# Kernel tuning notes

Measured on AMD Instinct MI355X. Metric: run time of the kernel, lower is better.

Reference implementation:

```python
import jax, jax.numpy as jnp
import numpy as np

B, S, I, H = 64, 512, 1024, 1024


def setup_inputs() -> dict:
    key = jax.random.key(0)
    ks = jax.random.split(key, 7)
    sc = 0.02
    return {
        "x": jax.random.normal(ks[0], (B, S, I), jnp.float32),
        "Wx0": jax.random.normal(ks[1], (I, 4 * H), jnp.float32) * sc,
        "Wh0": jax.random.normal(ks[2], (H, 4 * H), jnp.float32) * sc,
        "b0": jax.random.normal(ks[3], (4 * H,), jnp.float32) * sc,
        "Wx1": jax.random.normal(ks[4], (H, 4 * H), jnp.float32) * sc,
        "Wh1": jax.random.normal(ks[5], (H, 4 * H), jnp.float32) * sc,
        "b1": jax.random.normal(ks[6], (4 * H,), jnp.float32) * sc,
    }


def _lstm_layer(x_seq, Wx, Wh, b):
    """x_seq: (S, B, in). Gate order along 4H axis: i, f, g, o."""
    hid = Wh.shape[0]
    # Precompute input-side projections for all timesteps (one big GEMM).
    xg = jnp.einsum('sbi,ih->sbh', x_seq, Wx) + b  # (S, B, 4H)

    def step(carry, xg_t):
        h, c = carry
        g = xg_t + h @ Wh                      # (B, 4H)
        i, f, gg, o = jnp.split(g, 4, axis=-1)
        i = jax.nn.sigmoid(i)
        f = jax.nn.sigmoid(f)
        gg = jnp.tanh(gg)
        o = jax.nn.sigmoid(o)
        c = f * c + i * gg
        h = o * jnp.tanh(c)
        return (h, c), h

    bsz = x_seq.shape[1]
    h0 = jnp.zeros((bsz, hid), x_seq.dtype)
    c0 = jnp.zeros((bsz, hid), x_seq.dtype)
    (_, _), hs = jax.lax.scan(step, (h0, c0), xg)
    return hs  # (S, B, H)


def reference(x, Wx0, Wh0, b0, Wx1, Wh1, b1):
    # batch_first=True -> (B,S,I); internal layout is time-major (S,B,I)
    xs = jnp.swapaxes(x, 0, 1)
    h1 = _lstm_layer(xs, Wx0, Wh0, b0)
    h2 = _lstm_layer(h1, Wx1, Wh1, b1)
    return jnp.swapaxes(h2, 0, 1)  # (B, S, H)
```

## Files before the change

kernel.cpp:

```cpp
#include <hip/hip_runtime.h>
#include <hip/hip_bf16.h>

#define SEQ  512
#define HID  1024
#define G4   4096
#define NBLK 128

typedef short bf16x8 __attribute__((ext_vector_type(8)));
typedef float f32x4  __attribute__((ext_vector_type(4)));
typedef unsigned long long u64;

static __device__ __forceinline__ unsigned short f2b(float f) {
  union { float f; unsigned u; } v; v.f = f;
  unsigned r = (v.u + 0x7FFFu + ((v.u >> 16) & 1u)) >> 16;
  return (unsigned short)r;
}

__global__ __launch_bounds__(256) void k_castx(const float* __restrict__ x,
                                               unsigned short* __restrict__ xb) {
  int idx = blockIdx.x * 256 + threadIdx.x;
  int r = idx >> 8, kq = idx & 255;
  int b = r & 63, s = r >> 6;
  float4 v = *reinterpret_cast<const float4*>(x + ((size_t)b * SEQ + s) * HID + (size_t)kq * 4);
  ushort4 o;
  o.x = f2b(v.x); o.y = f2b(v.y); o.z = f2b(v.z); o.w = f2b(v.w);
  *reinterpret_cast<ushort4*>(xb + (size_t)r * HID + kq * 4) = o;
}

__global__ __launch_bounds__(256) void k_wtrans(const float* __restrict__ W,
                                                unsigned short* __restrict__ WT) {
  __shared__ float tls[32][33];
  int tile = blockIdx.x;
  int nt = tile & 127, kt = tile >> 7;
  int tx = threadIdx.x & 31, ty = threadIdx.x >> 5;
  int k0 = kt * 32, n0 = nt * 32;
  for (int i = 0; i < 4; ++i)
    tls[ty + 8 * i][tx] = W[(size_t)(k0 + ty + 8 * i) * G4 + n0 + tx];
  __syncthreads();
  for (int i = 0; i < 4; ++i)
    WT[(size_t)(n0 + ty + 8 * i) * HID + k0 + tx] = f2b(tls[tx][ty + 8 * i]);
}

static __device__ __forceinline__ void poll_flags128(unsigned* flags, unsigned tgt) {
  const int l = threadIdx.x & 63;
  unsigned* p0 = flags + l * 32;
  unsigned* p1 = flags + (64 + l) * 32;
  long sp = 0;
  for (;;) {
    unsigned v0 = __hip_atomic_load(p0, __ATOMIC_RELAXED, __HIP_MEMORY_SCOPE_AGENT);
    unsigned v1 = __hip_atomic_load(p1, __ATOMIC_RELAXED, __HIP_MEMORY_SCOPE_AGENT);
    if (__all((v0 >= tgt) && (v1 >= tgt))) break;
    if (++sp > 2000000L) break;
    __builtin_amdgcn_s_sleep(1);
  }
  asm volatile("" ::: "memory");
}

static __device__ __forceinline__ void lds_wait(int* f, int tgt) {
  long sp = 0;
  while (__hip_atomic_load(f, __ATOMIC_RELAXED, __HIP_MEMORY_SCOPE_WORKGROUP) < tgt) {
    if (++sp > 50000000L) break;
    __builtin_amdgcn_s_sleep(1);
  }
  asm volatile("" ::: "memory");
}

__global__ __launch_bounds__(512, 1) void k_scan2(
    const unsigned short* __restrict__ xb,
    const unsigned short* __restrict__ WxT0, const unsigned short* __restrict__ WhT0,
    const float* __restrict__ b0,
    const unsigned short* __restrict__ WxT1, const unsigned short* __restrict__ WhT1,
    const float* __restrict__ b1,
    unsigned short* __restrict__ h1,
    unsigned short* __restrict__ h2, int h2mod,
    float* __restrict__ out,
    unsigned* __restrict__ bars) {
  __shared__ unsigned short wlds[32 * 2048];
  __shared__ float x_lds[2][4][8][64];
  __shared__ unsigned lds_arr;
  __shared__ int hrdy, xrdy;

  const int bk  = blockIdx.x;
  const int layer = bk >> 7;
  const int nb  = bk & 127;
  const int tid = threadIdx.x;
  const int w   = tid >> 6;
  const int l   = tid & 63;
  const int lq  = l >> 4, lr = l & 15;
  const int rt  = w & 3;
  const bool is_h = (w >= 4);

  const unsigned short* WxT = layer ? WxT1 : WxT0;
  const unsigned short* WhT = layer ? WhT1 : WhT0;
  const float* bias = layer ? b1 : b0;
  const unsigned short* aseq = layer ? h1 : xb;
  unsigned short* hout = layer ? h2 : h1;
  const int hmod = layer ? h2mod : 512;
  float* fout = layer ? out : nullptr;
  unsigned* ownflags = bars + layer * 4096;
  unsigned* l0flags  = bars;
  unsigned* myflag   = ownflags + nb * 32;

  if (tid == 0) { lds_arr = 0; hrdy = 0; xrdy = 0; }

  {
    int c = tid >> 4, seg = tid & 15;
    int gate = c >> 3, nl = c & 7;
    int gcol = gate * 1024 + nb * 8 + nl;
    const unsigned short* sx = WxT + (size_t)gcol * HID;
    const unsigned short* sh = WhT + (size_t)gcol * HID;
    for (int j = 0; j < 16; ++j) {
      int kk = seg * 128 + j * 8;
      const unsigned short* src = (kk < 1024) ? (sx + kk) : (sh + kk - 1024);
      uint4 v = *reinterpret_cast<const uint4*>(src);
      int db = (c * 4096 + kk * 2) ^ ((c & 7) << 4);
      *reinterpret_cast<uint4*>(reinterpret_cast<char*>(wlds) + db) = v;
    }
  }

  char* wbase = reinterpret_cast<char*>(wlds);
  const int csw = (lr & 7) << 4;
  const int cb0 = (lr) * 4096 + lq * 16;
  const int cb1 = (16 + lr) * 4096 + lq * 16;

  float bias_c[2];
#pragma unroll
  for (int ct = 0; ct < 2; ++ct) {
    int col = ct * 16 + lr;
    bias_c[ct] = bias[(col >> 3) * 1024 + nb * 8 + (col & 7)];
  }

  float cst[4] = {0.f, 0.f, 0.f, 0.f};

  __syncthreads();
  if (is_h) __builtin_amdgcn_s_setprio(1);

  if (!is_h) {
    if (layer) poll_flags128(l0flags, 1u);
    const bf16x8* ax = reinterpret_cast<const bf16x8*>(aseq) + (size_t)(rt * 16 + lr) * 128 + lq;
    f32x4 acc[2][4] = {};
#pragma unroll 8
    for (int ks = 0; ks < 32; ++ks) {
      bf16x8 a  = ax[ks * 4];
      bf16x8 bb0 = *reinterpret_cast<const bf16x8*>(wbase + ((cb0 + ks * 64) ^ csw));
      bf16x8 bb1 = *reinterpret_cast<const bf16x8*>(wbase + ((cb1 + ks * 64) ^ csw));
      acc[0][ks & 3] = __builtin_amdgcn_mfma_f32_16x16x32_bf16(a, bb0, acc[0][ks & 3], 0, 0, 0);
      acc[1][ks & 3] = __builtin_amdgcn_mfma_f32_16x16x32_bf16(a, bb1, acc[1][ks & 3], 0, 0, 0);
    }
#pragma unroll
    for (int ct = 0; ct < 2; ++ct) {
      f32x4 s = (acc[ct][0] + acc[ct][1]) + (acc[ct][2] + acc[ct][3]);
      float bc = bias_c[ct];
      x_lds[0][w][ct * 4 + 0][l] = s.x + bc;
      x_lds[0][w][ct * 4 + 1][l] = s.y + bc;
      x_lds[0][w][ct * 4 + 2][l] = s.z + bc;
      x_lds[0][w][ct * 4 + 3][l] = s.w + bc;
    }
  }
  __syncthreads();

  for (int t = 0; t < SEQ; ++t) {
    if (!is_h) {
      if (t + 1 < SEQ) {
        if (layer) {
          if (w == 0) {
            poll_flags128(l0flags, (unsigned)(t + 2));
            __hip_atomic_store(&xrdy, t + 1, __ATOMIC_RELAXED, __HIP_MEMORY_SCOPE_WORKGROUP);
          } else {
            lds_wait(&xrdy, t + 1);
          }
        }
        const bf16x8* ax = reinterpret_cast<const bf16x8*>(aseq)
                           + ((size_t)(t + 1) * 64 + rt * 16 + lr) * 128 + lq;
        f32x4 acc[2][4] = {};
#pragma unroll 8
        for (int ks = 0; ks < 32; ++ks) {
          bf16x8 a  = ax[ks * 4];
          bf16x8 bb0 = *reinterpret_cast<const bf16x8*>(wbase + ((cb0 + ks * 64) ^ csw));
          bf16x8 bb1 = *reinterpret_cast<const bf16x8*>(wbase + ((cb1 + ks * 64) ^ csw));
          acc[0][ks & 3] = __builtin_amdgcn_mfma_f32_16x16x32_bf16(a, bb0, acc[0][ks & 3], 0, 0, 0);
          acc[1][ks & 3] = __builtin_amdgcn_mfma_f32_16x16x32_bf16(a, bb1, acc[1][ks & 3], 0, 0, 0);
        }
        int bn2 = (t + 1) & 1;
#pragma unroll
        for (int ct = 0; ct < 2; ++ct) {
          f32x4 s = (acc[ct][0] + acc[ct][1]) + (acc[ct][2] + acc[ct][3]);
          float bc = bias_c[ct];
          x_lds[bn2][w][ct * 4 + 0][l] = s.x + bc;
          x_lds[bn2][w][ct * 4 + 1][l] = s.y + bc;
          x_lds[bn2][w][ct * 4 + 2][l] = s.z + bc;
          x_lds[bn2][w][ct * 4 + 3][l] = s.w + bc;
        }
      }
    } else {
      const int bn = t & 1;
      f32x4 acc[2][4];
#pragma unroll
      for (int ct = 0; ct < 2; ++ct) {
        acc[ct][0] = f32x4{x_lds[bn][rt][ct * 4 + 0][l], x_lds[bn][rt][ct * 4 + 1][l],
                           x_lds[bn][rt][ct * 4 + 2][l], x_lds[bn][rt][ct * 4 + 3][l]};
        acc[ct][1] = f32x4{0.f, 0.f, 0.f, 0.f};
        acc[ct][2] = f32x4{0.f, 0.f, 0.f, 0.f};
        acc[ct][3] = f32x4{0.f, 0.f, 0.f, 0.f};
      }

      if (t > 0) {
        if (w == 4) {
          poll_flags128(ownflags, (unsigned)t);
          __hip_atomic_store(&hrdy, t, __ATOMIC_RELAXED, __HIP_MEMORY_SCOPE_WORKGROUP);
        } else {
          lds_wait(&hrdy, t);
        }
        const size_t hbase = (size_t)((t - 1) % hmod) * (64 * HID) + (size_t)(rt * 16 + lr) * HID;
        if (hmod != 4) {
          const bf16x8* hp = reinterpret_cast<const bf16x8*>(hout + hbase) + lq;
#pragma unroll 8
          for (int ks = 0; ks < 32; ++ks) {
            bf16x8 a = hp[ks * 4];
            bf16x8 bb0 = *reinterpret_cast<const bf16x8*>(wbase + ((cb0 + 2048 + ks * 64) ^ csw));
            bf16x8 bb1 = *reinterpret_cast<const bf16x8*>(wbase + ((cb1 + 2048 + ks * 64) ^ csw));
            acc[0][ks & 3] = __builtin_amdgcn_mfma_f32_16x16x32_bf16(a, bb0, acc[0][ks & 3], 0, 0, 0);
            acc[1][ks & 3] = __builtin_amdgcn_mfma_f32_16x16x32_bf16(a, bb1, acc[1][ks & 3], 0, 0, 0);
          }
        } else {
          const u64* hp = reinterpret_cast<const u64*>(hout + hbase) + lq * 2;
#pragma unroll 8
          for (int ks = 0; ks < 32; ++ks) {
            u64 q0 = __hip_atomic_load(hp + ks * 8,     __ATOMIC_RELAXED, __HIP_MEMORY_SCOPE_AGENT);
            u64 q1 = __hip_atomic_load(hp + ks * 8 + 1, __ATOMIC_RELAXED, __HIP_MEMORY_SCOPE_AGENT);
            union { u64 q[2]; bf16x8 v; } u; u.q[0] = q0; u.q[1] = q1;
            bf16x8 bb0 = *reinterpret_cast<const bf16x8*>(wbase + ((cb0 + 2048 + ks * 64) ^ csw));
            bf16x8 bb1 = *reinterpret_cast<const bf16x8*>(wbase + ((cb1 + 2048 + ks * 64) ^ csw));
            acc[0][ks & 3] = __builtin_amdgcn_mfma_f32_16x16x32_bf16(u.v, bb0, acc[0][ks & 3], 0, 0, 0);
            acc[1][ks & 3] = __builtin_amdgcn_mfma_f32_16x16x32_bf16(u.v, bb1, acc[1][ks & 3], 0, 0, 0);
          }
        }
      }

      f32x4 s0 = (acc[0][0] + acc[0][1]) + (acc[0][2] + acc[0][3]);
      f32x4 s1 = (acc[1][0] + acc[1][1]) + (acc[1][2] + acc[1][3]);
      float a0[4] = {s0.x, s0.y, s0.z, s0.w};
      float a1[4] = {s1.x, s1.y, s1.z, s1.w};
      float b0r[4], b1r[4];
#pragma unroll
      for (int r = 0; r < 4; ++r) {
        b0r[r] = __shfl_xor(a0[r], 8, 64);
        b1r[r] = __shfl_xor(a1[r], 8, 64);
      }
      const bool isX = ((l & 8) == 0);
      float hvf[4];
#pragma unroll
      for (int r = 0; r < 4; ++r) {
        float gi = isX ? a0[r] : b0r[r];
        float gf = isX ? b0r[r] : a0[r];
        float gg = isX ? a1[r] : b1r[r];
        float go = isX ? b1r[r] : a1[r];
        float ig = 1.f / (1.f + __expf(-gi));
        float fg = 1.f / (1.f + __expf(-gf));
        float e2 = __expf(2.f * gg);
        float gv = (e2 - 1.f) / (e2 + 1.f);
        float og = 1.f / (1.f + __expf(-go));
        cst[r] = fg * cst[r] + ig * gv;
        float e2c = __expf(2.f * cst[r]);
        hvf[r] = og * (e2c - 1.f) / (e2c + 1.f);
      }
      float hn[4];
#pragma unroll
      for (int r = 0; r < 4; ++r) hn[r] = __shfl_xor(hvf[r], 1, 64);
      const bool ev = ((l & 1) == 0);
      unsigned pk[4]; float he[4], ho[4];
#pragma unroll
      for (int r = 0; r < 4; ++r) {
        he[r] = ev ? hvf[r] : hn[r];
        ho[r] = ev ? hn[r] : hvf[r];
        pk[r] = (unsigned)f2b(he[r]) | ((unsigned)f2b(ho[r]) << 16);
      }
      const int sub = ((l >> 3) & 1) * 2 + (l & 1);
      unsigned pks = sub == 0 ? pk[0] : sub == 1 ? pk[1] : sub == 2 ? pk[2] : pk[3];
      const int row = rt * 16 + lq * 4 + sub;
      const int cp  = (lr & 7) >> 1;
      unsigned* hw = reinterpret_cast<unsigned*>(hout + (size_t)(t % hmod) * (64 * HID))
                     + (size_t)row * 512 + nb * 4 + cp;
      __hip_atomic_store(hw, pks, __ATOMIC_RELAXED, __HIP_MEMORY_SCOPE_AGENT);

      asm volatile("s_waitcnt vmcnt(0)" ::: "memory");
      if (l == 0) {
        atomicAdd(&lds_arr, 1u);
        if (w == 4) {
          long sp = 0;
          while (__hip_atomic_load(&lds_arr, __ATOMIC_RELAXED, __HIP_MEMORY_SCOPE_WORKGROUP)
                 < 4u * (unsigned)(t + 1)) {
            if (++sp > 50000000L) break;
            __builtin_amdgcn_s_sleep(1);
          }
          __hip_atomic_store(myflag, (unsigned)(t + 1), __ATOMIC_RELAXED, __HIP_MEMORY_SCOPE_AGENT);
        }
      }

      if (fout) {
        float hes = sub == 0 ? he[0] : sub == 1 ? he[1] : sub == 2 ? he[2] : he[3];
        float hos = sub == 0 ? ho[0] : sub == 1 ? ho[1] : sub == 2 ? ho[2] : ho[3];
        *reinterpret_cast<float2*>(fout + (size_t)row * (SEQ * HID) + (size_t)t * HID
                                   + nb * 8 + cp * 2) = make_float2(hes, hos);
      }
    }
    __syncthreads();
  }
}

extern "C" void kernel_launch(void* const* d_in, const int* in_sizes, int n_in,
                              void* d_out, int out_size, void* d_ws, size_t ws_size,
                              hipStream_t stream) {
  const float* x   = (const float*)d_in[0];
  const float* Wx0 = (const float*)d_in[1];
  const float* Wh0 = (const float*)d_in[2];
  const float* b0  = (const float*)d_in[3];
  const float* Wx1 = (const float*)d_in[4];
  const float* Wh1 = (const float*)d_in[5];
  const float* b1  = (const float*)d_in[6];
  float* out = (float*)d_out;
  char* ws = (char*)d_ws;

  unsigned short* xb   = (unsigned short*)(ws);
  unsigned short* h1   = (unsigned short*)(ws + 67108864);
  unsigned short* WxT0 = (unsigned short*)(ws + 134217728);
  unsigned short* WhT0 = (unsigned short*)(ws + 142606336);
  unsigned short* WxT1 = (unsigned short*)(ws + 150994944);
  unsigned short* WhT1 = (unsigned short*)(ws + 159383552);
  unsigned* bars       = (unsigned*)(ws + 167772160);
  unsigned short* h2   = (unsigned short*)(ws + 167804928);
  int h2mod = (ws_size >= (size_t)167804928 + 67108864) ? 512 : 4;

  hipMemsetAsync(bars, 0, 32768, stream);
  k_castx<<<32768, 256, 0, stream>>>(x, xb);
  k_wtrans<<<4096, 256, 0, stream>>>(Wx0, WxT0);
  k_wtrans<<<4096, 256, 0, stream>>>(Wh0, WhT0);
  k_wtrans<<<4096, 256, 0, stream>>>(Wx1, WxT1);
  k_wtrans<<<4096, 256, 0, stream>>>(Wh1, WhT1);
  k_scan2<<<2 * NBLK, 512, 0, stream>>>(xb, WxT0, WhT0, b0, WxT1, WhT1, b1,
                                        h1, h2, h2mod, out, bars);
}
```

Baseline: 4.788 ms.

## Retile recurrent MFMA per wave and move output stores to x-projection waves

Each wave now computes 32 batch rows by 16 gate columns instead of 16 rows by 32 columns. The weight columns in LDS are interleaved by gate, so the i/f/g/o values for a hidden unit sit in adjacent lanes and are gathered with xor-1/xor-2 shuffles. This halves the LDS weight reads per k-step but doubles the global reads of the h operand on the recurrent critical path. The fp32 output stores are taken off the h-waves: the x-projection waves re-read the previous step's bf16 h from global memory and write it out. As a result the output now carries bf16-rounded values.

New measurement: 8.915 ms. 1.86x slower.

```diff
diff --git a/kernel.cpp b/kernel.cpp
--- a/kernel.cpp
+++ b/kernel.cpp
@@ -14,6 +14,12 @@
   union { float f; unsigned u; } v; v.f = f;
   unsigned r = (v.u + 0x7FFFu + ((v.u >> 16) & 1u)) >> 16;
   return (unsigned short)r;
+}
+static __device__ __forceinline__ float b2f_lo(unsigned u) {
+  union { unsigned u; float f; } v; v.u = u << 16; return v.f;
+}
+static __device__ __forceinline__ float b2f_hi(unsigned u) {
+  union { unsigned u; float f; } v; v.u = u & 0xFFFF0000u; return v.f;
 }
 
 __global__ __launch_bounds__(256) void k_castx(const float* __restrict__ x,
@@ -87,7 +93,8 @@
   const int w   = tid >> 6;
   const int l   = tid & 63;
   const int lq  = l >> 4, lr = l & 15;
-  const int rt  = w & 3;
+  const int rt2 = (w >> 1) & 1;
+  const int ct  = w & 1;
   const bool is_h = (w >= 4);
 
   const unsigned short* WxT = layer ? WxT1 : WxT0;
@@ -105,8 +112,8 @@
 
   {
     int c = tid >> 4, seg = tid & 15;
-    int gate = c >> 3, nl = c & 7;
-    int gcol = gate * 1024 + nb * 8 + nl;
+    int gate = c & 3, hcl = c >> 2;
+    int gcol = gate * 1024 + nb * 8 + hcl;
     const unsigned short* sx = WxT + (size_t)gcol * HID;
     const unsigned short* sh = WhT + (size_t)gcol * HID;
     for (int j = 0; j < 16; ++j) {
@@ -119,48 +126,55 @@
   }
 
   char* wbase = reinterpret_cast<char*>(wlds);
-  const int csw = (lr & 7) << 4;
-  const int cb0 = (lr) * 4096 + lq * 16;
-  const int cb1 = (16 + lr) * 4096 + lq * 16;
-
-  float bias_c[2];
-#pragma unroll
-  for (int ct = 0; ct < 2; ++ct) {
-    int col = ct * 16 + lr;
-    bias_c[ct] = bias[(col >> 3) * 1024 + nb * 8 + (col & 7)];
-  }
-
-  float cst[4] = {0.f, 0.f, 0.f, 0.f};
+  const int c_w = ct * 16 + lr;
+  const int csw = (c_w & 7) << 4;
+  const int cb  = c_w * 4096 + lq * 16;
+  const int gate = lr & 3;
+  const int hcl  = ct * 4 + (lr >> 2);
+  const float bias_c = bias[gate * 1024 + nb * 8 + hcl];
+
+  float cst[8] = {0.f};
 
   __syncthreads();
   if (is_h) __builtin_amdgcn_s_setprio(1);
 
   if (!is_h) {
     if (layer) poll_flags128(l0flags, 1u);
-    const bf16x8* ax = reinterpret_cast<const bf16x8*>(aseq) + (size_t)(rt * 16 + lr) * 128 + lq;
+    const bf16x8* ax0 = reinterpret_cast<const bf16x8*>(aseq)
+                        + (size_t)(rt2 * 32 + lr) * 128 + lq;
+    const bf16x8* ax1 = ax0 + 16 * 128;
     f32x4 acc[2][4] = {};
 #pragma unroll 8
     for (int ks = 0; ks < 32; ++ks) {
-      bf16x8 a  = ax[ks * 4];
-      bf16x8 bb0 = *reinterpret_cast<const bf16x8*>(wbase + ((cb0 + ks * 64) ^ csw));
-      bf16x8 bb1 = *reinterpret_cast<const bf16x8*>(wbase + ((cb1 + ks * 64) ^ csw));
-      acc[0][ks & 3] = __builtin_amdgcn_mfma_f32_16x16x32_bf16(a, bb0, acc[0][ks & 3], 0, 0, 0);
-      acc[1][ks & 3] = __builtin_amdgcn_mfma_f32_16x16x32_bf16(a, bb1, acc[1][ks & 3], 0, 0, 0);
+      bf16x8 a0 = ax0[ks * 4];
+      bf16x8 a1 = ax1[ks * 4];
+      bf16x8 bb = *reinterpret_cast<const bf16x8*>(wbase + ((cb + ks * 64) ^ csw));
+      acc[0][ks & 3] = __builtin_amdgcn_mfma_f32_16x16x32_bf16(a0, bb, acc[0][ks & 3], 0, 0, 0);
+      acc[1][ks & 3] = __builtin_amdgcn_mfma_f32_16x16x32_bf16(a1, bb, acc[1][ks & 3], 0, 0, 0);
     }
 #pragma unroll
-    for (int ct = 0; ct < 2; ++ct) {
-      f32x4 s = (acc[ct][0] + acc[ct][1]) + (acc[ct][2] + acc[ct][3]);
-      float bc = bias_c[ct];
-      x_lds[0][w][ct * 4 + 0][l] = s.x + bc;
-      x_lds[0][w][ct * 4 + 1][l] = s.y + bc;
-      x_lds[0][w][ct * 4 + 2][l] = s.z + bc;
-      x_lds[0][w][ct * 4 + 3][l] = s.w + bc;
+    for (int ar = 0; ar < 2; ++ar) {
+      f32x4 s = (acc[ar][0] + acc[ar][1]) + (acc[ar][2] + acc[ar][3]);
+      x_lds[0][w][ar * 4 + 0][l] = s.x + bias_c;
+      x_lds[0][w][ar * 4 + 1][l] = s.y + bias_c;
+      x_lds[0][w][ar * 4 + 2][l] = s.z + bias_c;
+      x_lds[0][w][ar * 4 + 3][l] = s.w + bias_c;
     }
   }
   __syncthreads();
 
   for (int t = 0; t < SEQ; ++t) {
     if (!is_h) {
+      if (fout && t > 0) {
+        int tc = t - 1;
+        const unsigned* sp32 = reinterpret_cast<const unsigned*>(
+            hout + (size_t)(tc % hmod) * (64 * HID)) + (size_t)l * 512 + nb * 4 + (w & 3);
+        unsigned pv = (hmod == 4)
+            ? __hip_atomic_load(sp32, __ATOMIC_RELAXED, __HIP_MEMORY_SCOPE_AGENT)
+            : *sp32;
+        *reinterpret_cast<float2*>(fout + (size_t)l * (SEQ * HID) + (size_t)tc * HID
+                                   + nb * 8 + (w & 3) * 2) = make_float2(b2f_lo(pv), b2f_hi(pv));
+      }
       if (t + 1 < SEQ) {
         if (layer) {
           if (w == 0) {
@@ -170,38 +184,39 @@
             lds_wait(&xrdy, t + 1);
           }
         }
-        const bf16x8* ax = reinterpret_cast<const bf16x8*>(aseq)
-                           + ((size_t)(t + 1) * 64 + rt * 16 + lr) * 128 + lq;
+        const bf16x8* ax0 = reinterpret_cast<const bf16x8*>(aseq)
+                            + ((size_t)(t + 1) * 64 + rt2 * 32 + lr) * 128 + lq;
+        const bf16x8* ax1 = ax0 + 16 * 128;
         f32x4 acc[2][4] = {};
 #pragma unroll 8
         for (int ks = 0; ks < 32; ++ks) {
-          bf16x8 a  = ax[ks * 4];
-          bf16x8 bb0 = *reinterpret_cast<const bf16x8*>(wbase + ((cb0 + ks * 64) ^ csw));
-          bf16x8 bb1 = *reinterpret_cast<const bf16x8*>(wbase + ((cb1 + ks * 64) ^ csw));
-          acc[0][ks & 3] = __builtin_amdgcn_mfma_f32_16x16x32_bf16(a, bb0, acc[0][ks & 3], 0, 0, 0);
-          acc[1][ks & 3] = __builtin_amdgcn_mfma_f32_16x16x32_bf16(a, bb1, acc[1][ks & 3], 0, 0, 0);
+          bf16x8 a0 = ax0[ks * 4];
+          bf16x8 a1 = ax1[ks * 4];
+          bf16x8 bb = *reinterpret_cast<const bf16x8*>(wbase + ((cb + ks * 64) ^ csw));
+          acc[0][ks & 3] = __builtin_amdgcn_mfma_f32_16x16x32_bf16(a0, bb, acc[0][ks & 3], 0, 0, 0);
+          acc[1][ks & 3] = __builtin_amdgcn_mfma_f32_16x16x32_bf16(a1, bb, acc[1][ks & 3], 0, 0, 0);
         }
         int bn2 = (t + 1) & 1;
 #pragma unroll
-        for (int ct = 0; ct < 2; ++ct) {
-          f32x4 s = (acc[ct][0] + acc[ct][1]) + (acc[ct][2] + acc[ct][3]);
-          float bc = bias_c[ct];
-          x_lds[bn2][w][ct * 4 + 0][l] = s.x + bc;
-          x_lds[bn2][w][ct * 4 + 1][l] = s.y + bc;
-          x_lds[bn2][w][ct * 4 + 2][l] = s.z + bc;
-          x_lds[bn2][w][ct * 4 + 3][l] = s.w + bc;
+        for (int ar = 0; ar < 2; ++ar) {
+          f32x4 s = (acc[ar][0] + acc[ar][1]) + (acc[ar][2] + acc[ar][3]);
+          x_lds[bn2][w][ar * 4 + 0][l] = s.x + bias_c;
+          x_lds[bn2][w][ar * 4 + 1][l] = s.y + bias_c;
+          x_lds[bn2][w][ar * 4 + 2][l] = s.z + bias_c;
+          x_lds[bn2][w][ar * 4 + 3][l] = s.w + bias_c;
         }
       }
     } else {
       const int bn = t & 1;
+      const int hw = w - 4;
       f32x4 acc[2][4];
 #pragma unroll
-      for (int ct = 0; ct < 2; ++ct) {
-        acc[ct][0] = f32x4{x_lds[bn][rt][ct * 4 + 0][l], x_lds[bn][rt][ct * 4 + 1][l],
-                           x_lds[bn][rt][ct * 4 + 2][l], x_lds[bn][rt][ct * 4 + 3][l]};
-        acc[ct][1] = f32x4{0.f, 0.f, 0.f, 0.f};
-        acc[ct][2] = f32x4{0.f, 0.f, 0.f, 0.f};
-        acc[ct][3] = f32x4{0.f, 0.f, 0.f, 0.f};
+      for (int ar = 0; ar < 2; ++ar) {
+        acc[ar][0] = f32x4{x_lds[bn][hw][ar * 4 + 0][l], x_lds[bn][hw][ar * 4 + 1][l],
+                           x_lds[bn][hw][ar * 4 + 2][l], x_lds[bn][hw][ar * 4 + 3][l]};
+        acc[ar][1] = f32x4{0.f, 0.f, 0.f, 0.f};
+        acc[ar][2] = f32x4{0.f, 0.f, 0.f, 0.f};
+        acc[ar][3] = f32x4{0.f, 0.f, 0.f, 0.f};
       }
 
       if (t > 0) {
@@ -211,77 +226,89 @@
         } else {
           lds_wait(&hrdy, t);
         }
-        const size_t hbase = (size_t)((t - 1) % hmod) * (64 * HID) + (size_t)(rt * 16 + lr) * HID;
+        const size_t hbase = (size_t)((t - 1) % hmod) * (64 * HID);
         if (hmod != 4) {
-          const bf16x8* hp = reinterpret_cast<const bf16x8*>(hout + hbase) + lq;
+          const bf16x8* hp0 = reinterpret_cast<const bf16x8*>(hout + hbase)
+                              + (size_t)(rt2 * 32 + lr) * 128 + lq;
+          const bf16x8* hp1 = hp0 + 16 * 128;
 #pragma unroll 8
           for (int ks = 0; ks < 32; ++ks) {
-            bf16x8 a = hp[ks * 4];
-            bf16x8 bb0 = *reinterpret_cast<const bf16x8*>(wbase + ((cb0 + 2048 + ks * 64) ^ csw));
-            bf16x8 bb1 = *reinterpret_cast<const bf16x8*>(wbase + ((cb1 + 2048 + ks * 64) ^ csw));
-            acc[0][ks & 3] = __builtin_amdgcn_mfma_f32_16x16x32_bf16(a, bb0, acc[0][ks & 3], 0, 0, 0);
-            acc[1][ks & 3] = __builtin_amdgcn_mfma_f32_16x16x32_bf16(a, bb1, acc[1][ks & 3], 0, 0, 0);
+            bf16x8 a0 = hp0[ks * 4];
+            bf16x8 a1 = hp1[ks * 4];
+            bf16x8 bb = *reinterpret_cast<const bf16x8*>(wbase + ((cb + 2048 + ks * 64) ^ csw));
+            acc[0][ks & 3] = __builtin_amdgcn_mfma_f32_16x16x32_bf16(a0, bb, acc[0][ks & 3], 0, 0, 0);
+            acc[1][ks & 3] = __builtin_amdgcn_mfma_f32_16x16x32_bf16(a1, bb, acc[1][ks & 3], 0, 0, 0);
           }
         } else {
-          const u64* hp = reinterpret_cast<const u64*>(hout + hbase) + lq * 2;
+          const u64* hq0 = reinterpret_cast<const u64*>(hout + hbase)
+                           + (size_t)(rt2 * 32 + lr) * 256 + lq * 2;
+          const u64* hq1 = hq0 + 16 * 256;
 #pragma unroll 8
           for (int ks = 0; ks < 32; ++ks) {
-            u64 q0 = __hip_atomic_load(hp + ks * 8,     __ATOMIC_RELAXED, __HIP_MEMORY_SCOPE_AGENT);
-            u64 q1 = __hip_atomic_load(hp + ks * 8 + 1, __ATOMIC_RELAXED, __HIP_MEMORY_SCOPE_AGENT);
-            union { u64 q[2]; bf16x8 v; } u; u.q[0] = q0; u.q[1] = q1;
-            bf16x8 bb0 = *reinterpret_cast<const bf16x8*>(wbase + ((cb0 + 2048 + ks * 64) ^ csw));
-            bf16x8 bb1 = *reinterpret_cast<const bf16x8*>(wbase + ((cb1 + 2048 + ks * 64) ^ csw));
-            acc[0][ks & 3] = __builtin_amdgcn_mfma_f32_16x16x32_bf16(u.v, bb0, acc[0][ks & 3], 0, 0, 0);
-            acc[1][ks & 3] = __builtin_amdgcn_mfma_f32_16x16x32_bf16(u.v, bb1, acc[1][ks & 3], 0, 0, 0);
+            u64 q0 = __hip_atomic_load(hq0 + ks * 8,     __ATOMIC_RELAXED, __HIP_MEMORY_SCOPE_AGENT);
+            u64 q1 = __hip_atomic_load(hq0 + ks * 8 + 1, __ATOMIC_RELAXED, __HIP_MEMORY_SCOPE_AGENT);
+            u64 q2 = __hip_atomic_load(hq1 + ks * 8,     __ATOMIC_RELAXED, __HIP_MEMORY_SCOPE_AGENT);
+            u64 q3 = __hip_atomic_load(hq1 + ks * 8 + 1, __ATOMIC_RELAXED, __HIP_MEMORY_SCOPE_AGENT);
+            union { u64 q[2]; bf16x8 v; } u0; u0.q[0] = q0; u0.q[1] = q1;
+            union { u64 q[2]; bf16x8 v; } u1; u1.q[0] = q2; u1.q[1] = q3;
+            bf16x8 bb = *reinterpret_cast<const bf16x8*>(wbase + ((cb + 2048 + ks * 64) ^ csw));
+            acc[0][ks & 3] = __builtin_amdgcn_mfma_f32_16x16x32_bf16(u0.v, bb, acc[0][ks & 3], 0, 0, 0);
+            acc[1][ks & 3] = __builtin_amdgcn_mfma_f32_16x16x32_bf16(u1.v, bb, acc[1][ks & 3], 0, 0, 0);
           }
         }
       }
 
-      f32x4 s0 = (acc[0][0] + acc[0][1]) + (acc[0][2] + acc[0][3]);
-      f32x4 s1 = (acc[1][0] + acc[1][1]) + (acc[1][2] + acc[1][3]);
-      float a0[4] = {s0.x, s0.y, s0.z, s0.w};
-      float a1[4] = {s1.x, s1.y, s1.z, s1.w};
-      float b0r[4], b1r[4];
-#pragma unroll
-      for (int r = 0; r < 4; ++r) {
-        b0r[r] = __shfl_xor(a0[r], 8, 64);
-        b1r[r] = __shfl_xor(a1[r], 8, 64);
-      }
-      const bool isX = ((l & 8) == 0);
-      float hvf[4];
-#pragma unroll
-      for (int r = 0; r < 4; ++r) {
-        float gi = isX ? a0[r] : b0r[r];
-        float gf = isX ? b0r[r] : a0[r];
-        float gg = isX ? a1[r] : b1r[r];
-        float go = isX ? b1r[r] : a1[r];
-        float ig = 1.f / (1.f + __expf(-gi));
-        float fg = 1.f / (1.f + __expf(-gf));
-        float e2 = __expf(2.f * gg);
-        float gv = (e2 - 1.f) / (e2 + 1.f);
-        float og = 1.f / (1.f + __expf(-go));
-        cst[r] = fg * cst[r] + ig * gv;
-        float e2c = __expf(2.f * cst[r]);
-        hvf[r] = og * (e2c - 1.f) / (e2c + 1.f);
-      }
-      float hn[4];
-#pragma unroll
-      for (int r = 0; r < 4; ++r) hn[r] = __shfl_xor(hvf[r], 1, 64);
-      const bool ev = ((l & 1) == 0);
-      unsigned pk[4]; float he[4], ho[4];
-#pragma unroll
-      for (int r = 0; r < 4; ++r) {
-        he[r] = ev ? hvf[r] : hn[r];
-        ho[r] = ev ? hn[r] : hvf[r];
-        pk[r] = (unsigned)f2b(he[r]) | ((unsigned)f2b(ho[r]) << 16);
-      }
-      const int sub = ((l >> 3) & 1) * 2 + (l & 1);
-      unsigned pks = sub == 0 ? pk[0] : sub == 1 ? pk[1] : sub == 2 ? pk[2] : pk[3];
-      const int row = rt * 16 + lq * 4 + sub;
-      const int cp  = (lr & 7) >> 1;
-      unsigned* hw = reinterpret_cast<unsigned*>(hout + (size_t)(t % hmod) * (64 * HID))
-                     + (size_t)row * 512 + nb * 4 + cp;
-      __hip_atomic_store(hw, pks, __ATOMIC_RELAXED, __HIP_MEMORY_SCOPE_AGENT);
+      float hvf[2][4], hn4[2][4];
+#pragma unroll
+      for (int ar = 0; ar < 2; ++ar) {
+        f32x4 s = (acc[ar][0] + acc[ar][1]) + (acc[ar][2] + acc[ar][3]);
+        float sv[4] = {s.x, s.y, s.z, s.w};
+#pragma unroll
+        for (int r = 0; r < 4; ++r) {
+          float a  = sv[r];
+          float b  = __shfl_xor(a, 1, 64);
+          float c2 = __shfl_xor(a, 2, 64);
+          float d2 = __shfl_xor(b, 2, 64);
+          float u0g = (gate & 1) ? b : a;
+          float u1g = (gate & 1) ? a : b;
+          float u2g = (gate & 1) ? d2 : c2;
+          float u3g = (gate & 1) ? c2 : d2;
+          float gi = (gate & 2) ? u2g : u0g;
+          float gf = (gate & 2) ? u3g : u1g;
+          float gg = (gate & 2) ? u0g : u2g;
+          float go = (gate & 2) ? u1g : u3g;
+          float ig = 1.f / (1.f + __expf(-gi));
+          float fg = 1.f / (1.f + __expf(-gf));
+          float e2 = __expf(2.f * gg);
+          float gv = (e2 - 1.f) / (e2 + 1.f);
+          float og = 1.f / (1.f + __expf(-go));
+          float& cr = cst[ar * 4 + r];
+          cr = fg * cr + ig * gv;
+          float e2c = __expf(2.f * cr);
+          hvf[ar][r] = og * (e2c - 1.f) / (e2c + 1.f);
+        }
+      }
+#pragma unroll
+      for (int ar = 0; ar < 2; ++ar)
+#pragma unroll
+        for (int r = 0; r < 4; ++r)
+          hn4[ar][r] = __shfl_xor(hvf[ar][r], 4, 64);
+
+      unsigned* hw32 = reinterpret_cast<unsigned*>(hout + (size_t)(t % hmod) * (64 * HID));
+      if ((lr & 4) == 0) {
+        const int ucol = nb * 4 + ct * 2 + (lr >> 3);
+#pragma unroll
+        for (int ar = 0; ar < 2; ++ar) {
+          float hsel = gate == 0 ? hvf[ar][0] : gate == 1 ? hvf[ar][1]
+                     : gate == 2 ? hvf[ar][2] : hvf[ar][3];
+          float nsel = gate == 0 ? hn4[ar][0] : gate == 1 ? hn4[ar][1]
+                     : gate == 2 ? hn4[ar][2] : hn4[ar][3];
+          unsigned pk = (unsigned)f2b(hsel) | ((unsigned)f2b(nsel) << 16);
+          const int row = rt2 * 32 + ar * 16 + lq * 4 + gate;
+          __hip_atomic_store(hw32 + (size_t)row * 512 + ucol, pk,
+                             __ATOMIC_RELAXED, __HIP_MEMORY_SCOPE_AGENT);
+        }
+      }
 
       asm volatile("s_waitcnt vmcnt(0)" ::: "memory");
       if (l == 0) {
@@ -296,15 +323,18 @@
           __hip_atomic_store(myflag, (unsigned)(t + 1), __ATOMIC_RELAXED, __HIP_MEMORY_SCOPE_AGENT);
         }
       }
-
-      if (fout) {
-        float hes = sub == 0 ? he[0] : sub == 1 ? he[1] : sub == 2 ? he[2] : he[3];
-        float hos = sub == 0 ? ho[0] : sub == 1 ? ho[1] : sub == 2 ? ho[2] : ho[3];
-        *reinterpret_cast<float2*>(fout + (size_t)row * (SEQ * HID) + (size_t)t * HID
-                                   + nb * 8 + cp * 2) = make_float2(hes, hos);
-      }
     }
     __syncthreads();
+  }
+
+  if (!is_h && fout) {
+    const unsigned* sp32 = reinterpret_cast<const unsigned*>(
+        hout + (size_t)(511 % hmod) * (64 * HID)) + (size_t)l * 512 + nb * 4 + (w & 3);
+    unsigned pv = (hmod == 4)
+        ? __hip_atomic_load(sp32, __ATOMIC_RELAXED, __HIP_MEMORY_SCOPE_AGENT)
+        : *sp32;
+    *reinterpret_cast<float2*>(fout + (size_t)l * (SEQ * HID) + (size_t)511 * HID
+                               + nb * 8 + (w & 3) * 2) = make_float2(b2f_lo(pv), b2f_hi(pv));
   }
 }
 
```

## Replace per-step block barriers with per-tile LDS sequence flags and offload output stores

Applied to the files above, without the earlier changes.

Removes the per-timestep __syncthreads between the x-projection waves and the recurrent h waves. Each row tile now hands off through LDS sequence counters (xseq/hseq), so the two wave groups can run decoupled. The last arriving h wave publishes the global step flag through the atomicAdd return value, instead of wave 4 spinning on the counter. The fp32 output write is moved to the x-projection waves, which read back the bf16 h values, so the output is now rounded to bf16 precision. The spin waits drop s_sleep, which keeps the critical path shorter but makes the waiting waves compete harder for issue slots.

Result: slower. 5.209 ms (+8.8%).

```diff
diff --git a/kernel.cpp b/kernel.cpp
--- a/kernel.cpp
+++ b/kernel.cpp
@@ -14,6 +14,12 @@
   union { float f; unsigned u; } v; v.f = f;
   unsigned r = (v.u + 0x7FFFu + ((v.u >> 16) & 1u)) >> 16;
   return (unsigned short)r;
+}
+static __device__ __forceinline__ float b2f_lo(unsigned u) {
+  union { unsigned u; float f; } v; v.u = u << 16; return v.f;
+}
+static __device__ __forceinline__ float b2f_hi(unsigned u) {
+  union { unsigned u; float f; } v; v.u = u & 0xFFFF0000u; return v.f;
 }
 
 __global__ __launch_bounds__(256) void k_castx(const float* __restrict__ x,
@@ -56,13 +62,17 @@
   asm volatile("" ::: "memory");
 }
 
-static __device__ __forceinline__ void lds_wait(int* f, int tgt) {
+static __device__ __forceinline__ void lds_wait_u(unsigned* f, unsigned tgt) {
   long sp = 0;
-  while (__hip_atomic_load(f, __ATOMIC_RELAXED, __HIP_MEMORY_SCOPE_WORKGROUP) < tgt) {
+  while (__hip_atomic_load(f, __ATOMIC_ACQUIRE, __HIP_MEMORY_SCOPE_WORKGROUP) < tgt) {
     if (++sp > 50000000L) break;
-    __builtin_amdgcn_s_sleep(1);
   }
   asm volatile("" ::: "memory");
+}
+static __device__ __forceinline__ void seq_pub(unsigned* p, unsigned v, int lane) {
+  asm volatile("s_waitcnt lgkmcnt(0)" ::: "memory");
+  if (lane == 0)
+    __hip_atomic_store(p, v, __ATOMIC_RELAXED, __HIP_MEMORY_SCOPE_WORKGROUP);
 }
 
 __global__ __launch_bounds__(512, 1) void k_scan2(
@@ -78,7 +88,8 @@
   __shared__ unsigned short wlds[32 * 2048];
   __shared__ float x_lds[2][4][8][64];
   __shared__ unsigned lds_arr;
-  __shared__ int hrdy, xrdy;
+  __shared__ unsigned xseq[4], hseq[4];
+  __shared__ unsigned hrdy, xrdy;
 
   const int bk  = blockIdx.x;
   const int layer = bk >> 7;
@@ -102,6 +113,7 @@
   unsigned* myflag   = ownflags + nb * 32;
 
   if (tid == 0) { lds_arr = 0; hrdy = 0; xrdy = 0; }
+  if (tid < 4) { xseq[tid] = 0; hseq[tid] = 0; }
 
   {
     int c = tid >> 4, seg = tid & 15;
@@ -136,40 +148,42 @@
   if (is_h) __builtin_amdgcn_s_setprio(1);
 
   if (!is_h) {
-    if (layer) poll_flags128(l0flags, 1u);
-    const bf16x8* ax = reinterpret_cast<const bf16x8*>(aseq) + (size_t)(rt * 16 + lr) * 128 + lq;
-    f32x4 acc[2][4] = {};
+    {
+      if (layer) poll_flags128(l0flags, 1u);
+      const bf16x8* ax = reinterpret_cast<const bf16x8*>(aseq) + (size_t)(rt * 16 + lr) * 128 + lq;
+      f32x4 acc[2][4] = {};
 #pragma unroll 8
-    for (int ks = 0; ks < 32; ++ks) {
-      bf16x8 a  = ax[ks * 4];
-      bf16x8 bb0 = *reinterpret_cast<const bf16x8*>(wbase + ((cb0 + ks * 64) ^ csw));
-      bf16x8 bb1 = *reinterpret_cast<const bf16x8*>(wbase + ((cb1 + ks * 64) ^ csw));
-      acc[0][ks & 3] = __builtin_amdgcn_mfma_f32_16x16x32_bf16(a, bb0, acc[0][ks & 3], 0, 0, 0);
-      acc[1][ks & 3] = __builtin_amdgcn_mfma_f32_16x16x32_bf16(a, bb1, acc[1][ks & 3], 0, 0, 0);
-    }
-#pragma unroll
-    for (int ct = 0; ct < 2; ++ct) {
-      f32x4 s = (acc[ct][0] + acc[ct][1]) + (acc[ct][2] + acc[ct][3]);
-      float bc = bias_c[ct];
-      x_lds[0][w][ct * 4 + 0][l] = s.x + bc;
-      x_lds[0][w][ct * 4 + 1][l] = s.y + bc;
-      x_lds[0][w][ct * 4 + 2][l] = s.z + bc;
-      x_lds[0][w][ct * 4 + 3][l] = s.w + bc;
-    }
-  }
-  __syncthreads();
-
-  for (int t = 0; t < SEQ; ++t) {
-    if (!is_h) {
+      for (int ks = 0; ks < 32; ++ks) {
+        bf16x8 a  = ax[ks * 4];
+        bf16x8 bb0 = *reinterpret_cast<const bf16x8*>(wbase + ((cb0 + ks * 64) ^ csw));
+        bf16x8 bb1 = *reinterpret_cast<const bf16x8*>(wbase + ((cb1 + ks * 64) ^ csw));
+        acc[0][ks & 3] = __builtin_amdgcn_mfma_f32_16x16x32_bf16(a, bb0, acc[0][ks & 3], 0, 0, 0);
+        acc[1][ks & 3] = __builtin_amdgcn_mfma_f32_16x16x32_bf16(a, bb1, acc[1][ks & 3], 0, 0, 0);
+      }
+#pragma unroll
+      for (int ct = 0; ct < 2; ++ct) {
+        f32x4 s = (acc[ct][0] + acc[ct][1]) + (acc[ct][2] + acc[ct][3]);
+        float bc = bias_c[ct];
+        x_lds[0][rt][ct * 4 + 0][l] = s.x + bc;
+        x_lds[0][rt][ct * 4 + 1][l] = s.y + bc;
+        x_lds[0][rt][ct * 4 + 2][l] = s.z + bc;
+        x_lds[0][rt][ct * 4 + 3][l] = s.w + bc;
+      }
+      seq_pub(&xseq[rt], 1u, l);
+    }
+
+    for (int t = 0; t < SEQ; ++t) {
       if (t + 1 < SEQ) {
         if (layer) {
           if (w == 0) {
             poll_flags128(l0flags, (unsigned)(t + 2));
-            __hip_atomic_store(&xrdy, t + 1, __ATOMIC_RELAXED, __HIP_MEMORY_SCOPE_WORKGROUP);
+            __hip_atomic_store(&xrdy, (unsigned)(t + 1), __ATOMIC_RELAXED,
+                               __HIP_MEMORY_SCOPE_WORKGROUP);
           } else {
-            lds_wait(&xrdy, t + 1);
+            lds_wait_u(&xrdy, (unsigned)(t + 1));
           }
         }
+        lds_wait_u(&hseq[rt], (unsigned)t);
         const bf16x8* ax = reinterpret_cast<const bf16x8*>(aseq)
                            + ((size_t)(t + 1) * 64 + rt * 16 + lr) * 128 + lq;
         f32x4 acc[2][4] = {};
@@ -186,13 +200,33 @@
         for (int ct = 0; ct < 2; ++ct) {
           f32x4 s = (acc[ct][0] + acc[ct][1]) + (acc[ct][2] + acc[ct][3]);
           float bc = bias_c[ct];
-          x_lds[bn2][w][ct * 4 + 0][l] = s.x + bc;
-          x_lds[bn2][w][ct * 4 + 1][l] = s.y + bc;
-          x_lds[bn2][w][ct * 4 + 2][l] = s.z + bc;
-          x_lds[bn2][w][ct * 4 + 3][l] = s.w + bc;
-        }
-      }
-    } else {
+          x_lds[bn2][rt][ct * 4 + 0][l] = s.x + bc;
+          x_lds[bn2][rt][ct * 4 + 1][l] = s.y + bc;
+          x_lds[bn2][rt][ct * 4 + 2][l] = s.z + bc;
+          x_lds[bn2][rt][ct * 4 + 3][l] = s.w + bc;
+        }
+        seq_pub(&xseq[rt], (unsigned)(t + 2), l);
+      }
+      if (fout && t > 0) {
+        lds_wait_u(&lds_arr, 4u * (unsigned)t);
+        const unsigned* sp32 = reinterpret_cast<const unsigned*>(
+            hout + (size_t)((t - 1) % hmod) * (64 * HID)) + (size_t)l * 512 + nb * 4 + rt;
+        unsigned pv = __hip_atomic_load(sp32, __ATOMIC_RELAXED, __HIP_MEMORY_SCOPE_AGENT);
+        *reinterpret_cast<float2*>(fout + (size_t)l * (SEQ * HID) + (size_t)(t - 1) * HID
+                                   + nb * 8 + rt * 2) = make_float2(b2f_lo(pv), b2f_hi(pv));
+      }
+    }
+    if (fout) {
+      lds_wait_u(&lds_arr, 4u * (unsigned)SEQ);
+      const unsigned* sp32 = reinterpret_cast<const unsigned*>(
+          hout + (size_t)(511 % hmod) * (64 * HID)) + (size_t)l * 512 + nb * 4 + rt;
+      unsigned pv = __hip_atomic_load(sp32, __ATOMIC_RELAXED, __HIP_MEMORY_SCOPE_AGENT);
+      *reinterpret_cast<float2*>(fout + (size_t)l * (SEQ * HID) + (size_t)511 * HID
+                                 + nb * 8 + rt * 2) = make_float2(b2f_lo(pv), b2f_hi(pv));
+    }
+  } else {
+    for (int t = 0; t < SEQ; ++t) {
+      lds_wait_u(&xseq[rt], (unsigned)(t + 1));
       const int bn = t & 1;
       f32x4 acc[2][4];
 #pragma unroll
@@ -203,13 +237,15 @@
         acc[ct][2] = f32x4{0.f, 0.f, 0.f, 0.f};
         acc[ct][3] = f32x4{0.f, 0.f, 0.f, 0.f};
       }
+      seq_pub(&hseq[rt], (unsigned)(t + 1), l);
 
       if (t > 0) {
         if (w == 4) {
           poll_flags128(ownflags, (unsigned)t);
-          __hip_atomic_store(&hrdy, t, __ATOMIC_RELAXED, __HIP_MEMORY_SCOPE_WORKGROUP);
+          __hip_atomic_store(&hrdy, (unsigned)t, __ATOMIC_RELAXED,
+                             __HIP_MEMORY_SCOPE_WORKGROUP);
         } else {
-          lds_wait(&hrdy, t);
+          lds_wait_u(&hrdy, (unsigned)t);
         }
         const size_t hbase = (size_t)((t - 1) % hmod) * (64 * HID) + (size_t)(rt * 16 + lr) * HID;
         if (hmod != 4) {
@@ -268,12 +304,12 @@
 #pragma unroll
       for (int r = 0; r < 4; ++r) hn[r] = __shfl_xor(hvf[r], 1, 64);
       const bool ev = ((l & 1) == 0);
-      unsigned pk[4]; float he[4], ho[4];
+      unsigned pk[4];
 #pragma unroll
       for (int r = 0; r < 4; ++r) {
-        he[r] = ev ? hvf[r] : hn[r];
-        ho[r] = ev ? hn[r] : hvf[r];
-        pk[r] = (unsigned)f2b(he[r]) | ((unsigned)f2b(ho[r]) << 16);
+        float he = ev ? hvf[r] : hn[r];
+        float ho = ev ? hn[r] : hvf[r];
+        pk[r] = (unsigned)f2b(he) | ((unsigned)f2b(ho) << 16);
       }
       const int sub = ((l >> 3) & 1) * 2 + (l & 1);
       unsigned pks = sub == 0 ? pk[0] : sub == 1 ? pk[1] : sub == 2 ? pk[2] : pk[3];
@@ -285,26 +321,12 @@
 
       asm volatile("s_waitcnt vmcnt(0)" ::: "memory");
       if (l == 0) {
-        atomicAdd(&lds_arr, 1u);
-        if (w == 4) {
-          long sp = 0;
-          while (__hip_atomic_load(&lds_arr, __ATOMIC_RELAXED, __HIP_MEMORY_SCOPE_WORKGROUP)
-                 < 4u * (unsigned)(t + 1)) {
-            if (++sp > 50000000L) break;
-            __builtin_amdgcn_s_sleep(1);
-          }
-          __hip_atomic_store(myflag, (unsigned)(t + 1), __ATOMIC_RELAXED, __HIP_MEMORY_SCOPE_AGENT);
-        }
-      }
-
-      if (fout) {
-        float hes = sub == 0 ? he[0] : sub == 1 ? he[1] : sub == 2 ? he[2] : he[3];
-        float hos = sub == 0 ? ho[0] : sub == 1 ? ho[1] : sub == 2 ? ho[2] : ho[3];
-        *reinterpret_cast<float2*>(fout + (size_t)row * (SEQ * HID) + (size_t)t * HID
-                                   + nb * 8 + cp * 2) = make_float2(hes, hos);
-      }
-    }
-    __syncthreads();
+        unsigned pb = atomicAdd(&lds_arr, 1u);
+        if ((pb & 3) == 3)
+          __hip_atomic_store(myflag, (pb >> 2) + 1u, __ATOMIC_RELAXED,
+                             __HIP_MEMORY_SCOPE_AGENT);
+      }
+    }
   }
 }
 
```

## Streamline per-step handshakes and move output stores off the recurrent critical path

Applied to the files above, without the earlier changes.

Every wave in the block now polls the global per-block flags itself, replacing the scheme where one wave polled and relayed readiness to the others through LDS. The per-step flag is published by whichever h-wave arrives last at the LDS counter, instead of wave 4 spinning until all four have arrived. The fp32 output write moves from the h-waves to the x-projection waves. Those waves read back the previous step's bf16 h and widen it with nontemporal stores, which takes global stores off the recurrence path. In exchange, the output is now bf16-rounded rather than full fp32, and there is more global polling traffic.

After: 5.429 ms. 13.4% more time.

```diff
diff --git a/kernel.cpp b/kernel.cpp
--- a/kernel.cpp
+++ b/kernel.cpp
@@ -8,12 +8,19 @@
 
 typedef short bf16x8 __attribute__((ext_vector_type(8)));
 typedef float f32x4  __attribute__((ext_vector_type(4)));
+typedef float f32x2  __attribute__((ext_vector_type(2)));
 typedef unsigned long long u64;
 
 static __device__ __forceinline__ unsigned short f2b(float f) {
   union { float f; unsigned u; } v; v.f = f;
   unsigned r = (v.u + 0x7FFFu + ((v.u >> 16) & 1u)) >> 16;
   return (unsigned short)r;
+}
+static __device__ __forceinline__ float b2f_lo(unsigned u) {
+  union { unsigned u; float f; } v; v.u = u << 16; return v.f;
+}
+static __device__ __forceinline__ float b2f_hi(unsigned u) {
+  union { unsigned u; float f; } v; v.u = u & 0xFFFF0000u; return v.f;
 }
 
 __global__ __launch_bounds__(256) void k_castx(const float* __restrict__ x,
@@ -51,15 +58,6 @@
     unsigned v1 = __hip_atomic_load(p1, __ATOMIC_RELAXED, __HIP_MEMORY_SCOPE_AGENT);
     if (__all((v0 >= tgt) && (v1 >= tgt))) break;
     if (++sp > 2000000L) break;
-    __builtin_amdgcn_s_sleep(1);
-  }
-  asm volatile("" ::: "memory");
-}
-
-static __device__ __forceinline__ void lds_wait(int* f, int tgt) {
-  long sp = 0;
-  while (__hip_atomic_load(f, __ATOMIC_RELAXED, __HIP_MEMORY_SCOPE_WORKGROUP) < tgt) {
-    if (++sp > 50000000L) break;
     __builtin_amdgcn_s_sleep(1);
   }
   asm volatile("" ::: "memory");
@@ -78,7 +76,6 @@
   __shared__ unsigned short wlds[32 * 2048];
   __shared__ float x_lds[2][4][8][64];
   __shared__ unsigned lds_arr;
-  __shared__ int hrdy, xrdy;
 
   const int bk  = blockIdx.x;
   const int layer = bk >> 7;
@@ -101,7 +98,7 @@
   unsigned* l0flags  = bars;
   unsigned* myflag   = ownflags + nb * 32;
 
-  if (tid == 0) { lds_arr = 0; hrdy = 0; xrdy = 0; }
+  if (tid == 0) lds_arr = 0;
 
   {
     int c = tid >> 4, seg = tid & 15;
@@ -161,15 +158,17 @@
 
   for (int t = 0; t < SEQ; ++t) {
     if (!is_h) {
+      if (fout && t > 0) {
+        const unsigned* sp32 = reinterpret_cast<const unsigned*>(
+            hout + (size_t)((t - 1) % hmod) * (64 * HID)) + (size_t)l * 512 + nb * 4 + rt;
+        unsigned pv = __hip_atomic_load(sp32, __ATOMIC_RELAXED, __HIP_MEMORY_SCOPE_AGENT);
+        f32x2 o2; o2.x = b2f_lo(pv); o2.y = b2f_hi(pv);
+        __builtin_nontemporal_store(o2,
+            reinterpret_cast<f32x2*>(fout + (size_t)l * (SEQ * HID) + (size_t)(t - 1) * HID
+                                     + nb * 8 + rt * 2));
+      }
       if (t + 1 < SEQ) {
-        if (layer) {
-          if (w == 0) {
-            poll_flags128(l0flags, (unsigned)(t + 2));
-            __hip_atomic_store(&xrdy, t + 1, __ATOMIC_RELAXED, __HIP_MEMORY_SCOPE_WORKGROUP);
-          } else {
-            lds_wait(&xrdy, t + 1);
-          }
-        }
+        if (layer) poll_flags128(l0flags, (unsigned)(t + 2));
         const bf16x8* ax = reinterpret_cast<const bf16x8*>(aseq)
                            + ((size_t)(t + 1) * 64 + rt * 16 + lr) * 128 + lq;
         f32x4 acc[2][4] = {};
@@ -205,12 +204,7 @@
       }
 
       if (t > 0) {
-        if (w == 4) {
-          poll_flags128(ownflags, (unsigned)t);
-          __hip_atomic_store(&hrdy, t, __ATOMIC_RELAXED, __HIP_MEMORY_SCOPE_WORKGROUP);
-        } else {
-          lds_wait(&hrdy, t);
-        }
+        poll_flags128(ownflags, (unsigned)t);
         const size_t hbase = (size_t)((t - 1) % hmod) * (64 * HID) + (size_t)(rt * 16 + lr) * HID;
         if (hmod != 4) {
           const bf16x8* hp = reinterpret_cast<const bf16x8*>(hout + hbase) + lq;
@@ -268,12 +262,12 @@
 #pragma unroll
       for (int r = 0; r < 4; ++r) hn[r] = __shfl_xor(hvf[r], 1, 64);
       const bool ev = ((l & 1) == 0);
-      unsigned pk[4]; float he[4], ho[4];
+      unsigned pk[4];
 #pragma unroll
       for (int r = 0; r < 4; ++r) {
-        he[r] = ev ? hvf[r] : hn[r];
-        ho[r] = ev ? hn[r] : hvf[r];
-        pk[r] = (unsigned)f2b(he[r]) | ((unsigned)f2b(ho[r]) << 16);
+        float he = ev ? hvf[r] : hn[r];
+        float ho = ev ? hn[r] : hvf[r];
+        pk[r] = (unsigned)f2b(he) | ((unsigned)f2b(ho) << 16);
       }
       const int sub = ((l >> 3) & 1) * 2 + (l & 1);
       unsigned pks = sub == 0 ? pk[0] : sub == 1 ? pk[1] : sub == 2 ? pk[2] : pk[3];
@@ -285,26 +279,23 @@
 
       asm volatile("s_waitcnt vmcnt(0)" ::: "memory");
       if (l == 0) {
-        atomicAdd(&lds_arr, 1u);
-        if (w == 4) {
-          long sp = 0;
-          while (__hip_atomic_load(&lds_arr, __ATOMIC_RELAXED, __HIP_MEMORY_SCOPE_WORKGROUP)
-                 < 4u * (unsigned)(t + 1)) {
-            if (++sp > 50000000L) break;
-            __builtin_amdgcn_s_sleep(1);
-          }
-          __hip_atomic_store(myflag, (unsigned)(t + 1), __ATOMIC_RELAXED, __HIP_MEMORY_SCOPE_AGENT);
-        }
-      }
-
-      if (fout) {
-        float hes = sub == 0 ? he[0] : sub == 1 ? he[1] : sub == 2 ? he[2] : he[3];
-        float hos = sub == 0 ? ho[0] : sub == 1 ? ho[1] : sub == 2 ? ho[2] : ho[3];
-        *reinterpret_cast<float2*>(fout + (size_t)row * (SEQ * HID) + (size_t)t * HID
-                                   + nb * 8 + cp * 2) = make_float2(hes, hos);
+        unsigned pb = atomicAdd(&lds_arr, 1u);
+        if ((pb & 3) == 3)
+          __hip_atomic_store(myflag, (pb >> 2) + 1u, __ATOMIC_RELAXED,
+                             __HIP_MEMORY_SCOPE_AGENT);
       }
     }
     __syncthreads();
+  }
+
+  if (!is_h && fout) {
+    const unsigned* sp32 = reinterpret_cast<const unsigned*>(
+        hout + (size_t)(511 % hmod) * (64 * HID)) + (size_t)l * 512 + nb * 4 + rt;
+    unsigned pv = __hip_atomic_load(sp32, __ATOMIC_RELAXED, __HIP_MEMORY_SCOPE_AGENT);
+    f32x2 o2; o2.x = b2f_lo(pv); o2.y = b2f_hi(pv);
+    __builtin_nontemporal_store(o2,
+        reinterpret_cast<f32x2*>(fout + (size_t)l * (SEQ * HID) + (size_t)511 * HID
+                                 + nb * 8 + rt * 2));
   }
 }
 
@@ -331,7 +322,7 @@
   unsigned short* h2   = (unsigned short*)(ws + 167804928);
   int h2mod = (ws_size >= (size_t)167804928 + 67108864) ? 512 : 4;
 
-  hipMemsetAsync(bars, 0, 32768, stream);
+  (void)hipMemsetAsync(bars, 0, 32768, stream);
   k_castx<<<32768, 256, 0, stream>>>(x, xb);
   k_wtrans<<<4096, 256, 0, stream>>>(Wx0, WxT0);
   k_wtrans<<<4096, 256, 0, stream>>>(Wh0, WhT0);
```
